# Kernel tuning notes

Hardware: AMD Instinct MI355X
Metric: run time of the kernel (lower is better)

## Reference

```python
import jax, jax.numpy as jnp
import numpy as np

N = 50000   # nodes
E = 800000  # edges (avg degree 16)
H = 3       # attention heads
D_IN, D_HID, D_OUT = 256, 64, 10


def setup_inputs() -> dict:
    key = jax.random.key(0)
    ks = jax.random.split(key, 8)
    x = jax.random.normal(ks[0], (N, D_IN), dtype=jnp.float32)
    edge_index = jax.random.randint(ks[1], (2, E), 0, N, dtype=jnp.int64)
    W1 = jax.random.normal(ks[2], (H, D_IN, D_HID), dtype=jnp.float32) / np.sqrt(D_IN)
    a_src1 = jax.random.normal(ks[3], (H, D_HID), dtype=jnp.float32) / np.sqrt(D_HID)
    a_dst1 = jax.random.normal(ks[4], (H, D_HID), dtype=jnp.float32) / np.sqrt(D_HID)
    W2 = jax.random.normal(ks[5], (H, D_HID, D_OUT), dtype=jnp.float32) / np.sqrt(D_HID)
    a_src2 = jax.random.normal(ks[6], (H, D_OUT), dtype=jnp.float32) / np.sqrt(D_OUT)
    a_dst2 = jax.random.normal(ks[7], (H, D_OUT), dtype=jnp.float32) / np.sqrt(D_OUT)
    return {"x": x, "edge_index": edge_index, "W1": W1, "a_src1": a_src1,
            "a_dst1": a_dst1, "W2": W2, "a_src2": a_src2, "a_dst2": a_dst2}


def gat_layer(x, src, dst, W, a_s, a_d, n):
    # x: [N, Din]; W: [H, Din, Dout]; returns [N, Dout] (heads averaged)
    z = jnp.einsum('nd,hde->nhe', x, W)                     # [N, H, Dout]
    e_src = jnp.einsum('nhe,he->nh', z, a_s)[src]           # [E, H]
    e_dst = jnp.einsum('nhe,he->nh', z, a_d)[dst]           # [E, H]
    e = jax.nn.leaky_relu(e_src + e_dst, 0.2)               # [E, H]
    # numerically-stable softmax over incoming edges of each dst node
    m = jax.lax.stop_gradient(jax.ops.segment_max(e, dst, num_segments=n))
    ex = jnp.exp(e - m[dst])                                # [E, H]
    denom = jax.ops.segment_sum(ex, dst, num_segments=n)    # [N, H]
    alpha = ex / (denom[dst] + 1e-16)                       # [E, H]
    out = jax.ops.segment_sum(z[src] * alpha[:, :, None], dst, num_segments=n)
    return out.mean(axis=1)                                 # [N, Dout]


def reference(x, edge_index, W1, a_src1, a_dst1, W2, a_src2, a_dst2):
    n = x.shape[0]
    src, dst = edge_index[0], edge_index[1]
    # dropout layers are identity in eval/deterministic mode
    h = gat_layer(x, src, dst, W1, a_src1, a_dst1, n)
    h = jax.nn.elu(h)
    h = gat_layer(h, src, dst, W2, a_src2, a_dst2, n)
    return h, jax.nn.log_softmax(h, axis=1)
```

## Files before the change

kernel.cpp:

```cpp
#include <hip/hip_runtime.h>
#include <math.h>

#define DIN  256
#define DHID 64
#define NH   3
#define DOUT 10
#define CAP  64

typedef __attribute__((ext_vector_type(8))) short bf16x8;
typedef __attribute__((ext_vector_type(4))) float f32x4;

__device__ inline unsigned short f2bf(float f) {
    unsigned u = __builtin_bit_cast(unsigned, f);
    unsigned r = (u + 0x7FFFu + ((u >> 16) & 1u)) >> 16;
    return (unsigned short)r;
}
__device__ inline float bf2f(unsigned short s) {
    unsigned u = ((unsigned)s) << 16;
    return __builtin_bit_cast(float, u);
}
__device__ inline f32x4 cvt4(ushort4 z) {
    f32x4 r;
    r[0] = bf2f(z.x); r[1] = bf2f(z.y); r[2] = bf2f(z.z); r[3] = bf2f(z.w);
    return r;
}


__global__ __launch_bounds__(256) void repack_zero_kernel(const float* __restrict__ W1,
                                                          const float* __restrict__ W2,
                                                          unsigned short* __restrict__ W1p,
                                                          float* __restrict__ W2cat,
                                                          int* __restrict__ cursor, int N) {
    int bid = blockIdx.x;
    int tid = threadIdx.x;
    int nzb = (N + 255) >> 8;
    if (bid < 192) {
        int idx = bid * 256 + tid;
        int j = idx & 7, l = (idx >> 3) & 63, q = (idx >> 9) & 7, t = idx >> 12;
        int c = t * 16 + (l & 15);
        int k = q * 32 + (l >> 4) * 8 + j;
        int h = c >> 6, jj = c & 63;
        W1p[idx] = f2bf(W1[h * 16384 + k * 64 + jj]);
    } else if (bid < 192 + nzb) {
        int i = (bid - 192) * 256 + tid;
        if (i < N) cursor[i] = 0;
    } else {
        int idx = (bid - 192 - nzb) * 256 + tid;
        if (idx < 2048) {
            int kk = idx >> 5, c = idx & 31;
            float wv = 0.f;
            if (c < 30) {
                int h = c / 10, j = c % 10;
                wv = W2[(h * 64 + kk) * 10 + j];
            }
            W2cat[idx] = wv;
        }
    }
}


#define SCHUNK 2048

__global__ __launch_bounds__(256) void scatter_kernel(const int* __restrict__ src,
                                                      const int* __restrict__ dst,
                                                      int* __restrict__ cursor,
                                                      unsigned short* __restrict__ esrcp,
                                                      int E, int pbase) {
    int part = blockIdx.x & 7;
    int base = (blockIdx.x >> 3) * SCHUNK;
    int tid = threadIdx.x;
    int lo = part * pbase, hi = lo + pbase;
    #pragma unroll
    for (int k = 0; k < SCHUNK / 256; ++k) {
        int i = base + k * 256 + tid;
        if (i < E) {
            int d = dst[i];
            int s = src[i];
            if (d >= lo && d < hi) {
                int pos = atomicAdd(cursor + d, 1);
                if (pos < CAP) esrcp[d * CAP + pos] = (unsigned short)s;
            }
        }
    }
}


__global__ __launch_bounds__(128) void gemm1_mfma_kernel(const float* __restrict__ x,
                                                         const bf16x8* __restrict__ W1p,
                                                         const float* __restrict__ a_s,
                                                         const float* __restrict__ a_d,
                                                         unsigned short* __restrict__ z1bf,
                                                         float* __restrict__ s1,
                                                         float* __restrict__ d1, int n) {
    __shared__ unsigned short Xs[32][272];
    int tid = threadIdx.x;
    int w = tid >> 6, lane = tid & 63;
    int m = lane & 15, quad = lane >> 4;
    int n0 = blockIdx.x * 32;

    for (int i = tid; i < 2048; i += 128) {
        int r = i >> 6, c4 = i & 63;
        int nn = n0 + r;
        float4 a = (nn < n) ? *(const float4*)(x + (size_t)nn * 256 + c4 * 4)
                            : (float4){0.f, 0.f, 0.f, 0.f};
        ushort4 b;
        b.x = f2bf(a.x); b.y = f2bf(a.y); b.z = f2bf(a.z); b.w = f2bf(a.w);
        *(ushort4*)(&Xs[r][c4 * 4]) = b;
    }
    __syncthreads();

    int rloc = w * 16 + m;
    f32x4 acc[12];
    #pragma unroll
    for (int t = 0; t < 12; ++t) acc[t] = (f32x4){0.f, 0.f, 0.f, 0.f};
    #pragma unroll
    for (int q = 0; q < 8; ++q) {
        bf16x8 af = *(const bf16x8*)(&Xs[rloc][q * 32 + quad * 8]);
        #pragma unroll
        for (int t = 0; t < 12; ++t) {
            bf16x8 bfr = W1p[(t * 8 + q) * 64 + lane];
            acc[t] = __builtin_amdgcn_mfma_f32_16x16x32_bf16(af, bfr, acc[t], 0, 0, 0);
        }
    }
    __syncthreads();

    float as_r[12], ad_r[12];
    #pragma unroll
    for (int t = 0; t < 12; ++t) { as_r[t] = a_s[t * 16 + m]; ad_r[t] = a_d[t * 16 + m]; }

    #pragma unroll
    for (int reg = 0; reg < 4; ++reg) {
        int row_loc = w * 16 + quad * 4 + reg;
        int row_out = n0 + row_loc;
        bool ok = row_out < n;
        float ps[3] = {0.f, 0.f, 0.f}, pd[3] = {0.f, 0.f, 0.f};
        #pragma unroll
        for (int t = 0; t < 12; ++t) {
            float v = acc[t][reg];
            Xs[row_loc][t * 16 + m] = f2bf(v);
            ps[t >> 2] += v * as_r[t];
            pd[t >> 2] += v * ad_r[t];
        }
        #pragma unroll
        for (int h = 0; h < 3; ++h) {
            float s = ps[h], d = pd[h];
            #pragma unroll
            for (int msk = 1; msk < 16; msk <<= 1) {
                s += __shfl_xor(s, msk, 16);
                d += __shfl_xor(d, msk, 16);
            }
            if (ok && m == 0) { s1[row_out * 4 + h] = s; d1[row_out * 4 + h] = d; }
        }
    }
    __syncthreads();

    for (int i = tid; i < 1536; i += 128) {
        int r = i / 48, c4 = i % 48;
        int nn = n0 + r;
        if (nn < n)
            *(ushort4*)(z1bf + (size_t)nn * 192 + c4 * 4) = *(const ushort4*)(&Xs[r][c4 * 4]);
    }
}


__global__ __launch_bounds__(256) void agg1_gemm2_kernel(
        const int* __restrict__ cnts, const unsigned short* __restrict__ esrcp,
        const float* __restrict__ s1, const float* __restrict__ d1,
        const unsigned short* __restrict__ z1bf,
        const float* __restrict__ W2cat, const float* __restrict__ as2,
        const float* __restrict__ ad2,
        unsigned short* __restrict__ z2bf,
        float* __restrict__ s2, float* __restrict__ d2, int n) {
    __shared__ float Ws[64][32];
    __shared__ float wlds[4][196];
    __shared__ float hb[4][64];
    __shared__ float tb[4][64];
    int tid = threadIdx.x;
    int lane = tid & 63, wave = tid >> 6;

    for (int idx = tid; idx < 1024; idx += 256)
        ((float2*)&Ws[0][0])[idx] = ((const float2*)W2cat)[idx];
    __syncthreads();

    int v = blockIdx.x * 4 + wave;
    if (v >= n) return;
    int cnt = cnts[v]; if (cnt > CAP) cnt = CAP;
    int m16 = lane & 15;
    int grp = lane >> 4;
    int head = grp > 2 ? 2 : grp;
    bool rowact = lane < 48;
    float dv0 = d1[v * 4], dv1 = d1[v * 4 + 1], dv2 = d1[v * 4 + 2];
    float* wl = wlds[wave];

    int u_l = 0; float w0 = 0.f, w1 = 0.f, w2 = 0.f;
    if (lane < cnt) {
        u_l = (int)esrcp[v * CAP + lane];
        float4 sv = *(const float4*)(s1 + (size_t)u_l * 4);
        float e0 = sv.x + dv0; e0 = e0 > 0.f ? e0 : 0.2f * e0;
        float e1 = sv.y + dv1; e1 = e1 > 0.f ? e1 : 0.2f * e1;
        float e2 = sv.z + dv2; e2 = e2 > 0.f ? e2 : 0.2f * e2;
        w0 = __expf(e0); w1 = __expf(e1); w2 = __expf(e2);
    }
    wl[lane] = w0; wl[65 + lane] = w1; wl[130 + lane] = w2;

    f32x4 acc = (f32x4){0.f, 0.f, 0.f, 0.f};
    if (rowact) {
        int rnd = (cnt + 7) & ~7;
        const int wb = head * 65;
        ushort4 zr[8]; float wr[8];
        #pragma unroll
        for (int i = 0; i < 8; ++i) {
            int u = __builtin_amdgcn_readlane(u_l, i);
            zr[i] = *(const ushort4*)(z1bf + (size_t)u * 192 + lane * 4);
            wr[i] = wl[wb + i];
        }
        for (int j = 8; j < rnd; j += 8) {
            ushort4 zn[8]; float wn[8];
            #pragma unroll
            for (int i = 0; i < 8; ++i) {
                int u = __builtin_amdgcn_readlane(u_l, j + i);
                zn[i] = *(const ushort4*)(z1bf + (size_t)u * 192 + lane * 4);
                wn[i] = wl[wb + j + i];
            }
            #pragma unroll
            for (int i = 0; i < 8; ++i) acc += cvt4(zr[i]) * wr[i];
            #pragma unroll
            for (int i = 0; i < 8; ++i) { zr[i] = zn[i]; wr[i] = wn[i]; }
        }
        #pragma unroll
        for (int i = 0; i < 8; ++i) acc += cvt4(zr[i]) * wr[i];
    }

    float4 wv4 = *(const float4*)(&wl[head * 65 + m16 * 4]);
    float denp = wv4.x + wv4.y + wv4.z + wv4.w;
    #pragma unroll
    for (int msk = 1; msk < 16; msk <<= 1) denp += __shfl_xor(denp, msk, 16);

    float invd = (1.f / 3.f) / (denp + 1e-16f);
    float acc0 = rowact ? acc[0] * invd : 0.f;
    float acc1 = rowact ? acc[1] * invd : 0.f;
    float acc2 = rowact ? acc[2] * invd : 0.f;
    float acc3 = rowact ? acc[3] * invd : 0.f;
    acc0 += __shfl_down(acc0, 32, 64); acc0 += __shfl_down(acc0, 16, 64);
    acc1 += __shfl_down(acc1, 32, 64); acc1 += __shfl_down(acc1, 16, 64);
    acc2 += __shfl_down(acc2, 32, 64); acc2 += __shfl_down(acc2, 16, 64);
    acc3 += __shfl_down(acc3, 32, 64); acc3 += __shfl_down(acc3, 16, 64);
    if (lane < 16) {
        float4 o;
        o.x = acc0 > 0.f ? acc0 : __expf(acc0) - 1.f;
        o.y = acc1 > 0.f ? acc1 : __expf(acc1) - 1.f;
        o.z = acc2 > 0.f ? acc2 : __expf(acc2) - 1.f;
        o.w = acc3 > 0.f ? acc3 : __expf(acc3) - 1.f;
        *(float4*)(&hb[wave][lane * 4]) = o;
    }

    int c = lane & 31, half = lane >> 5;
    int k0 = half * 32;
    float zc0 = 0.f, zc1 = 0.f;
    #pragma unroll
    for (int k = 0; k < 32; k += 2) {
        zc0 += hb[wave][k0 + k]     * Ws[k0 + k][c];
        zc1 += hb[wave][k0 + k + 1] * Ws[k0 + k + 1][c];
    }
    float zc = zc0 + zc1;
    zc += __shfl_down(zc, 32, 64);
    if (lane < 32) {
        z2bf[(size_t)v * 32 + c] = f2bf(zc);
        if (c < 30) {
            tb[wave][c]      = zc * as2[c];
            tb[wave][32 + c] = zc * ad2[c];
        }
    }
    if (lane < 6) {
        int h = lane >> 1;
        int base = (lane & 1) * 32 + h * 10;
        float sum = 0.f;
        #pragma unroll
        for (int j = 0; j < 10; ++j) sum += tb[wave][base + j];
        if ((lane & 1) == 0) s2[v * 4 + h] = sum;
        else                 d2[v * 4 + h] = sum;
    }
}


__global__ __launch_bounds__(256) void agg2_kernel(const int* __restrict__ cnts,
                                                   const unsigned short* __restrict__ esrcp,
                                                   const float* __restrict__ s2,
                                                   const float* __restrict__ d2,
                                                   const unsigned short* __restrict__ z2bf,
                                                   float* __restrict__ out, int n) {
    __shared__ float wlds[4][196];
    __shared__ float dlds[4][4];
    int tid = threadIdx.x;
    int lane = tid & 63, wave = tid >> 6;
    int v = blockIdx.x * 4 + wave;
    if (v >= n) return;
    int cnt = cnts[v]; if (cnt > CAP) cnt = CAP;
    int c2 = lane & 15;
    int quad = lane >> 4;
    int headc = c2 < 5 ? 0 : (c2 < 10 ? 1 : 2);
    int headg = quad > 2 ? 2 : quad;
    float dv0 = d2[v * 4], dv1 = d2[v * 4 + 1], dv2 = d2[v * 4 + 2];
    float* wl = wlds[wave];

    int u_l = 0; float w0 = 0.f, w1 = 0.f, w2 = 0.f;
    if (lane < cnt) {
        u_l = (int)esrcp[v * CAP + lane];
        float4 sv = *(const float4*)(s2 + (size_t)u_l * 4);
        float e0 = sv.x + dv0; e0 = e0 > 0.f ? e0 : 0.2f * e0;
        float e1 = sv.y + dv1; e1 = e1 > 0.f ? e1 : 0.2f * e1;
        float e2 = sv.z + dv2; e2 = e2 > 0.f ? e2 : 0.2f * e2;
        w0 = __expf(e0); w1 = __expf(e1); w2 = __expf(e2);
    }
    wl[lane] = w0; wl[65 + lane] = w1; wl[130 + lane] = w2;

    float ax = 0.f, ay = 0.f;
    {
        int rnd = (cnt + 7) & ~7;
        const int wb = headc * 65;
        int ua = __shfl(u_l, quad, 64);
        int ub = __shfl(u_l, 4 + quad, 64);
        float wa = wl[wb + quad], wbb = wl[wb + 4 + quad];
        ushort2 za = *(const ushort2*)(z2bf + (size_t)ua * 32 + c2 * 2);
        ushort2 zb = *(const ushort2*)(z2bf + (size_t)ub * 32 + c2 * 2);
        for (int j = 8; j < rnd; j += 8) {
            int un1 = __shfl(u_l, j + quad, 64);
            int un2 = __shfl(u_l, j + 4 + quad, 64);
            float wn1 = wl[wb + j + quad], wn2 = wl[wb + j + 4 + quad];
            ushort2 zn1 = *(const ushort2*)(z2bf + (size_t)un1 * 32 + c2 * 2);
            ushort2 zn2 = *(const ushort2*)(z2bf + (size_t)un2 * 32 + c2 * 2);
            ax += wa * bf2f(za.x) + wbb * bf2f(zb.x);
            ay += wa * bf2f(za.y) + wbb * bf2f(zb.y);
            wa = wn1; wbb = wn2; za = zn1; zb = zn2;
        }
        ax += wa * bf2f(za.x) + wbb * bf2f(zb.x);
        ay += wa * bf2f(za.y) + wbb * bf2f(zb.y);
    }

    float4 wv = *(const float4*)(&wl[headg * 65 + c2 * 4]);
    float denp = wv.x + wv.y + wv.z + wv.w;
    #pragma unroll
    for (int msk = 1; msk < 16; msk <<= 1) denp += __shfl_xor(denp, msk, 16);
    if (c2 == 0 && quad < 3) dlds[wave][quad] = denp;
    float den = dlds[wave][headc];

    ax += __shfl_down(ax, 32, 64); ax += __shfl_down(ax, 16, 64);
    ay += __shfl_down(ay, 32, 64); ay += __shfl_down(ay, 16, 64);
    float inv = 1.f / (den + 1e-16f);
    float rx = ax * inv, ry = ay * inv;
    float rx5  = __shfl(rx, lane + 5, 64);
    float rx10 = __shfl(rx, lane + 10, 64);
    float ry5  = __shfl(ry, lane + 5, 64);
    float ry10 = __shfl(ry, lane + 10, 64);
    float rrx = (rx + rx5 + rx10) * (1.f / 3.f);
    float rry = (ry + ry5 + ry10) * (1.f / 3.f);
    bool act = lane < 5;
    float mx = act ? fmaxf(rrx, rry) : -1e30f;
    #pragma unroll
    for (int msk = 1; msk < 8; msk <<= 1) mx = fmaxf(mx, __shfl_xor(mx, msk, 8));
    float e = act ? (__expf(rrx - mx) + __expf(rry - mx)) : 0.f;
    #pragma unroll
    for (int msk = 1; msk < 8; msk <<= 1) e += __shfl_xor(e, msk, 8);
    float lg = __logf(e);
    if (act) {
        float2 o1; o1.x = rrx; o1.y = rry;
        float2 o2; o2.x = rrx - mx - lg; o2.y = rry - mx - lg;
        *(float2*)(out + (size_t)v * DOUT + c2 * 2) = o1;
        *(float2*)(out + (size_t)n * DOUT + (size_t)v * DOUT + c2 * 2) = o2;
    }
}


extern "C" void kernel_launch(void* const* d_in, const int* in_sizes, int n_in,
                              void* d_out, int out_size, void* d_ws, size_t ws_size,
                              hipStream_t stream) {
    const float* x   = (const float*)d_in[0];
    const int*   ei  = (const int*)d_in[1];
    const float* W1  = (const float*)d_in[2];
    const float* as1 = (const float*)d_in[3];
    const float* ad1 = (const float*)d_in[4];
    const float* W2  = (const float*)d_in[5];
    const float* as2 = (const float*)d_in[6];
    const float* ad2 = (const float*)d_in[7];
    float* out = (float*)d_out;

    const int N = in_sizes[0] / DIN;
    const int E = in_sizes[1] / 2;
    const int* src = ei;
    const int* dst = ei + E;

    char* p = (char*)d_ws;
    auto alloc = [&](size_t bytes) -> void* {
        void* r = (void*)p;
        p += (bytes + 255) & ~(size_t)255;
        return r;
    };
    int* cursor  = (int*)alloc((size_t)N * 4);
    unsigned short* esrcp = (unsigned short*)alloc((size_t)N * CAP * 2);
    unsigned short* W1p  = (unsigned short*)alloc((size_t)49152 * 2);
    float* W2cat = (float*)alloc((size_t)2048 * 4);
    unsigned short* z1bf = (unsigned short*)alloc((size_t)N * 192 * 2);
    float* s1    = (float*)alloc((size_t)N * 4 * 4);
    float* d1    = (float*)alloc((size_t)N * 4 * 4);
    unsigned short* z2bf = (unsigned short*)alloc((size_t)N * 32 * 2);
    float* s2    = (float*)alloc((size_t)N * 4 * 4);
    float* d2    = (float*)alloc((size_t)N * 4 * 4);
    (void)alloc(512);

    int nzb = (N + 255) / 256;
    repack_zero_kernel<<<192 + nzb + 8, 256, 0, stream>>>(W1, W2, W1p, W2cat, cursor, N);

    int pbase = (N + 7) / 8;
    int nchunks = (E + SCHUNK - 1) / SCHUNK;
    scatter_kernel<<<nchunks * 8, 256, 0, stream>>>(src, dst, cursor, esrcp, E, pbase);

    gemm1_mfma_kernel<<<(N + 31) / 32, 128, 0, stream>>>(x, (const bf16x8*)W1p, as1, ad1,
                                                         z1bf, s1, d1, N);
    agg1_gemm2_kernel<<<(N + 3) / 4, 256, 0, stream>>>(cursor, esrcp, s1, d1, z1bf,
                                                       W2cat, as2, ad2, z2bf, s2, d2, N);
    agg2_kernel<<<(N + 3) / 4, 256, 0, stream>>>(cursor, esrcp, s2, d2, z2bf, out, N);
}
```

Baseline: 248.6 us.

## Deepen gather prefetch in agg1 and keep transposed W2 in registers

The fused layer-1 aggregation and layer-2 GEMM kernel now issues the first 16 neighbour-row gathers before computing the attention weights, and keeps two batches of 8 in flight instead of one. It also drops the per-block shared-memory staging of W2 and its __syncthreads, loading a transposed W2 layout straight into registers as float4 vectors. The per-wave weight buffer is padded to a 68-float stride so weights can be read as vector loads. In exchange register pressure rises and every node now processes at least 16 neighbour slots, even when it has fewer.

```diff
diff --git a/kernel.cpp b/kernel.cpp
--- a/kernel.cpp
+++ b/kernel.cpp
@@ -29,7 +29,7 @@
 __global__ __launch_bounds__(256) void repack_zero_kernel(const float* __restrict__ W1,
                                                           const float* __restrict__ W2,
                                                           unsigned short* __restrict__ W1p,
-                                                          float* __restrict__ W2cat,
+                                                          float* __restrict__ W2catT,
                                                           int* __restrict__ cursor, int N) {
     int bid = blockIdx.x;
     int tid = threadIdx.x;
@@ -47,13 +47,13 @@
     } else {
         int idx = (bid - 192 - nzb) * 256 + tid;
         if (idx < 2048) {
-            int kk = idx >> 5, c = idx & 31;
+            int cc = idx >> 6, kk = idx & 63;
             float wv = 0.f;
-            if (c < 30) {
-                int h = c / 10, j = c % 10;
+            if (cc < 30) {
+                int h = cc / 10, j = cc % 10;
                 wv = W2[(h * 64 + kk) * 10 + j];
             }
-            W2cat[idx] = wv;
+            W2catT[idx] = wv;
         }
     }
 }
@@ -163,76 +163,94 @@
 }
 
 
+#define CONSUME8(Z, OFF)                                              \
+    {                                                                 \
+        f32x4 wa4 = *(const f32x4*)(&wl[wb + (OFF)]);                 \
+        f32x4 wb4 = *(const f32x4*)(&wl[wb + (OFF) + 4]);             \
+        acc += cvt4(Z[0]) * wa4[0]; acc += cvt4(Z[1]) * wa4[1];       \
+        acc += cvt4(Z[2]) * wa4[2]; acc += cvt4(Z[3]) * wa4[3];       \
+        acc += cvt4(Z[4]) * wb4[0]; acc += cvt4(Z[5]) * wb4[1];       \
+        acc += cvt4(Z[6]) * wb4[2]; acc += cvt4(Z[7]) * wb4[3];       \
+    }
+
 __global__ __launch_bounds__(256) void agg1_gemm2_kernel(
         const int* __restrict__ cnts, const unsigned short* __restrict__ esrcp,
         const float* __restrict__ s1, const float* __restrict__ d1,
         const unsigned short* __restrict__ z1bf,
-        const float* __restrict__ W2cat, const float* __restrict__ as2,
+        const float* __restrict__ W2catT, const float* __restrict__ as2,
         const float* __restrict__ ad2,
         unsigned short* __restrict__ z2bf,
         float* __restrict__ s2, float* __restrict__ d2, int n) {
-    __shared__ float Ws[64][32];
-    __shared__ float wlds[4][196];
+    __shared__ float wlds[4][204];
     __shared__ float hb[4][64];
     __shared__ float tb[4][64];
     int tid = threadIdx.x;
     int lane = tid & 63, wave = tid >> 6;
-
-    for (int idx = tid; idx < 1024; idx += 256)
-        ((float2*)&Ws[0][0])[idx] = ((const float2*)W2cat)[idx];
-    __syncthreads();
-
     int v = blockIdx.x * 4 + wave;
     if (v >= n) return;
     int cnt = cnts[v]; if (cnt > CAP) cnt = CAP;
     int m16 = lane & 15;
     int grp = lane >> 4;
     int head = grp > 2 ? 2 : grp;
+    int c = lane & 31, half = lane >> 5;
     bool rowact = lane < 48;
+    const int wb = head * 68;
+    float* wl = wlds[wave];
+
+    int u_l = 0;
+    if (lane < cnt) u_l = (int)esrcp[v * CAP + lane];
+
+    ushort4 zA[8], zB[8];
+    if (rowact) {
+        #pragma unroll
+        for (int i = 0; i < 8; ++i) {
+            int u = __builtin_amdgcn_readlane(u_l, i);
+            zA[i] = *(const ushort4*)(z1bf + (size_t)u * 192 + lane * 4);
+        }
+        #pragma unroll
+        for (int i = 0; i < 8; ++i) {
+            int u = __builtin_amdgcn_readlane(u_l, 8 + i);
+            zB[i] = *(const ushort4*)(z1bf + (size_t)u * 192 + lane * 4);
+        }
+    }
+
+    f32x4 wsr[8];
+    #pragma unroll
+    for (int j2 = 0; j2 < 8; ++j2)
+        wsr[j2] = *(const f32x4*)(W2catT + (c << 6) + (half << 5) + (j2 << 2));
+
     float dv0 = d1[v * 4], dv1 = d1[v * 4 + 1], dv2 = d1[v * 4 + 2];
-    float* wl = wlds[wave];
-
-    int u_l = 0; float w0 = 0.f, w1 = 0.f, w2 = 0.f;
+    float w0 = 0.f, w1 = 0.f, w2 = 0.f;
     if (lane < cnt) {
-        u_l = (int)esrcp[v * CAP + lane];
         float4 sv = *(const float4*)(s1 + (size_t)u_l * 4);
         float e0 = sv.x + dv0; e0 = e0 > 0.f ? e0 : 0.2f * e0;
         float e1 = sv.y + dv1; e1 = e1 > 0.f ? e1 : 0.2f * e1;
         float e2 = sv.z + dv2; e2 = e2 > 0.f ? e2 : 0.2f * e2;
         w0 = __expf(e0); w1 = __expf(e1); w2 = __expf(e2);
     }
-    wl[lane] = w0; wl[65 + lane] = w1; wl[130 + lane] = w2;
-
+    wl[lane] = w0; wl[68 + lane] = w1; wl[136 + lane] = w2;
+
+    int rnd = (cnt + 7) & ~7; if (rnd < 16) rnd = 16;
     f32x4 acc = (f32x4){0.f, 0.f, 0.f, 0.f};
     if (rowact) {
-        int rnd = (cnt + 7) & ~7;
-        const int wb = head * 65;
-        ushort4 zr[8]; float wr[8];
-        #pragma unroll
-        for (int i = 0; i < 8; ++i) {
-            int u = __builtin_amdgcn_readlane(u_l, i);
-            zr[i] = *(const ushort4*)(z1bf + (size_t)u * 192 + lane * 4);
-            wr[i] = wl[wb + i];
-        }
-        for (int j = 8; j < rnd; j += 8) {
-            ushort4 zn[8]; float wn[8];
+        int jc = 0;
+        for (int js = 16; js < rnd; js += 8) {
+            ushort4 zN[8];
             #pragma unroll
             for (int i = 0; i < 8; ++i) {
-                int u = __builtin_amdgcn_readlane(u_l, j + i);
-                zn[i] = *(const ushort4*)(z1bf + (size_t)u * 192 + lane * 4);
-                wn[i] = wl[wb + j + i];
+                int u = __builtin_amdgcn_readlane(u_l, js + i);
+                zN[i] = *(const ushort4*)(z1bf + (size_t)u * 192 + lane * 4);
             }
+            CONSUME8(zA, jc); jc += 8;
             #pragma unroll
-            for (int i = 0; i < 8; ++i) acc += cvt4(zr[i]) * wr[i];
-            #pragma unroll
-            for (int i = 0; i < 8; ++i) { zr[i] = zn[i]; wr[i] = wn[i]; }
-        }
-        #pragma unroll
-        for (int i = 0; i < 8; ++i) acc += cvt4(zr[i]) * wr[i];
-    }
-
-    float4 wv4 = *(const float4*)(&wl[head * 65 + m16 * 4]);
-    float denp = wv4.x + wv4.y + wv4.z + wv4.w;
+            for (int i = 0; i < 8; ++i) { zA[i] = zB[i]; zB[i] = zN[i]; }
+        }
+        CONSUME8(zA, jc);
+        CONSUME8(zB, jc + 8);
+    }
+
+    f32x4 wv4 = *(const f32x4*)(&wl[head * 68 + m16 * 4]);
+    float denp = wv4[0] + wv4[1] + wv4[2] + wv4[3];
     #pragma unroll
     for (int msk = 1; msk < 16; msk <<= 1) denp += __shfl_xor(denp, msk, 16);
 
@@ -254,15 +272,13 @@
         *(float4*)(&hb[wave][lane * 4]) = o;
     }
 
-    int c = lane & 31, half = lane >> 5;
-    int k0 = half * 32;
-    float zc0 = 0.f, zc1 = 0.f;
-    #pragma unroll
-    for (int k = 0; k < 32; k += 2) {
-        zc0 += hb[wave][k0 + k]     * Ws[k0 + k][c];
-        zc1 += hb[wave][k0 + k + 1] * Ws[k0 + k + 1][c];
-    }
-    float zc = zc0 + zc1;
+    f32x4 accW = (f32x4){0.f, 0.f, 0.f, 0.f};
+    #pragma unroll
+    for (int j2 = 0; j2 < 8; ++j2) {
+        f32x4 h4 = *(const f32x4*)(&hb[wave][(half << 5) + (j2 << 2)]);
+        accW += h4 * wsr[j2];
+    }
+    float zc = accW[0] + accW[1] + accW[2] + accW[3];
     zc += __shfl_down(zc, 32, 64);
     if (lane < 32) {
         z2bf[(size_t)v * 32 + c] = f2bf(zc);
@@ -398,7 +414,7 @@
     int* cursor  = (int*)alloc((size_t)N * 4);
     unsigned short* esrcp = (unsigned short*)alloc((size_t)N * CAP * 2);
     unsigned short* W1p  = (unsigned short*)alloc((size_t)49152 * 2);
-    float* W2cat = (float*)alloc((size_t)2048 * 4);
+    float* W2catT = (float*)alloc((size_t)2048 * 4);
     unsigned short* z1bf = (unsigned short*)alloc((size_t)N * 192 * 2);
     float* s1    = (float*)alloc((size_t)N * 4 * 4);
     float* d1    = (float*)alloc((size_t)N * 4 * 4);
@@ -408,7 +424,7 @@
     (void)alloc(512);
 
     int nzb = (N + 255) / 256;
-    repack_zero_kernel<<<192 + nzb + 8, 256, 0, stream>>>(W1, W2, W1p, W2cat, cursor, N);
+    repack_zero_kernel<<<192 + nzb + 8, 256, 0, stream>>>(W1, W2, W1p, W2catT, cursor, N);
 
     int pbase = (N + 7) / 8;
     int nchunks = (E + SCHUNK - 1) / SCHUNK;
@@ -417,6 +433,6 @@
     gemm1_mfma_kernel<<<(N + 31) / 32, 128, 0, stream>>>(x, (const bf16x8*)W1p, as1, ad1,
                                                          z1bf, s1, d1, N);
     agg1_gemm2_kernel<<<(N + 3) / 4, 256, 0, stream>>>(cursor, esrcp, s1, d1, z1bf,
-                                                       W2cat, as2, ad2, z2bf, s2, d2, N);
+                                                       W2catT, as2, ad2, z2bf, s2, d2, N);
     agg2_kernel<<<(N + 3) / 4, 256, 0, stream>>>(cursor, esrcp, s2, d2, z2bf, out, N);
 }
```

Result: slower. 275.6 us (+10.9%).

## Split each node's layer-1 aggregation across two waves and combine via LDS

Applied to the files above, without the earlier changes.

The layer-1 aggregation kernel now gives each destination node two waves, each gathering half of its incoming edges. The second wave writes its partial accumulators and softmax denominator to shared memory, and the first wave combines them and runs the fused ELU plus second-layer projection. This doubles the grid and halves the per-wave serial gather chain, exposing more memory-level parallelism at the cost of a block barrier and an idle half-wave during the epilogue. The scatter kernel also loads src only for edges that fall in the block's partition.

```diff
diff --git a/kernel.cpp b/kernel.cpp
--- a/kernel.cpp
+++ b/kernel.cpp
@@ -75,8 +75,8 @@
         int i = base + k * 256 + tid;
         if (i < E) {
             int d = dst[i];
-            int s = src[i];
             if (d >= lo && d < hi) {
+                int s = src[i];
                 int pos = atomicAdd(cursor + d, 1);
                 if (pos < CAP) esrcp[d * CAP + pos] = (unsigned short)s;
             }
@@ -172,41 +172,46 @@
         unsigned short* __restrict__ z2bf,
         float* __restrict__ s2, float* __restrict__ d2, int n) {
     __shared__ float Ws[64][32];
-    __shared__ float wlds[4][196];
-    __shared__ float hb[4][64];
-    __shared__ float tb[4][64];
+    __shared__ float wlds[4][102];
+    __shared__ float accb[2][200];
+    __shared__ float hb[2][64];
+    __shared__ float tb[2][64];
     int tid = threadIdx.x;
     int lane = tid & 63, wave = tid >> 6;
 
     for (int idx = tid; idx < 1024; idx += 256)
         ((float2*)&Ws[0][0])[idx] = ((const float2*)W2cat)[idx];
-    __syncthreads();
-
-    int v = blockIdx.x * 4 + wave;
-    if (v >= n) return;
+
+    int pairid = wave >> 1;
+    int hf = wave & 1;
+    int v = blockIdx.x * 2 + pairid;
+    if (v >= n) v = n - 1;
     int cnt = cnts[v]; if (cnt > CAP) cnt = CAP;
+    int cnt2 = (cnt + 1) >> 1;
+    int myoff = hf * cnt2;
+    int mycnt = hf ? (cnt - cnt2) : cnt2;
     int m16 = lane & 15;
     int grp = lane >> 4;
     int head = grp > 2 ? 2 : grp;
     bool rowact = lane < 48;
+    const int wb = head * 34;
+    float* wl = wlds[wave];
+
     float dv0 = d1[v * 4], dv1 = d1[v * 4 + 1], dv2 = d1[v * 4 + 2];
-    float* wl = wlds[wave];
-
     int u_l = 0; float w0 = 0.f, w1 = 0.f, w2 = 0.f;
-    if (lane < cnt) {
-        u_l = (int)esrcp[v * CAP + lane];
+    if (lane < mycnt) {
+        u_l = (int)esrcp[v * CAP + myoff + lane];
         float4 sv = *(const float4*)(s1 + (size_t)u_l * 4);
         float e0 = sv.x + dv0; e0 = e0 > 0.f ? e0 : 0.2f * e0;
         float e1 = sv.y + dv1; e1 = e1 > 0.f ? e1 : 0.2f * e1;
         float e2 = sv.z + dv2; e2 = e2 > 0.f ? e2 : 0.2f * e2;
         w0 = __expf(e0); w1 = __expf(e1); w2 = __expf(e2);
     }
-    wl[lane] = w0; wl[65 + lane] = w1; wl[130 + lane] = w2;
+    if (lane < 32) { wl[lane] = w0; wl[34 + lane] = w1; wl[68 + lane] = w2; }
 
     f32x4 acc = (f32x4){0.f, 0.f, 0.f, 0.f};
     if (rowact) {
-        int rnd = (cnt + 7) & ~7;
-        const int wb = head * 65;
+        int rnd = (mycnt + 7) & ~7;
         ushort4 zr[8]; float wr[8];
         #pragma unroll
         for (int i = 0; i < 8; ++i) {
@@ -231,54 +236,63 @@
         for (int i = 0; i < 8; ++i) acc += cvt4(zr[i]) * wr[i];
     }
 
-    float4 wv4 = *(const float4*)(&wl[head * 65 + m16 * 4]);
-    float denp = wv4.x + wv4.y + wv4.z + wv4.w;
+    float2 dpr = *(const float2*)(&wl[head * 34 + m16 * 2]);
+    float denp = dpr.x + dpr.y;
     #pragma unroll
     for (int msk = 1; msk < 16; msk <<= 1) denp += __shfl_xor(denp, msk, 16);
 
-    float invd = (1.f / 3.f) / (denp + 1e-16f);
-    float acc0 = rowact ? acc[0] * invd : 0.f;
-    float acc1 = rowact ? acc[1] * invd : 0.f;
-    float acc2 = rowact ? acc[2] * invd : 0.f;
-    float acc3 = rowact ? acc[3] * invd : 0.f;
-    acc0 += __shfl_down(acc0, 32, 64); acc0 += __shfl_down(acc0, 16, 64);
-    acc1 += __shfl_down(acc1, 32, 64); acc1 += __shfl_down(acc1, 16, 64);
-    acc2 += __shfl_down(acc2, 32, 64); acc2 += __shfl_down(acc2, 16, 64);
-    acc3 += __shfl_down(acc3, 32, 64); acc3 += __shfl_down(acc3, 16, 64);
-    if (lane < 16) {
-        float4 o;
-        o.x = acc0 > 0.f ? acc0 : __expf(acc0) - 1.f;
-        o.y = acc1 > 0.f ? acc1 : __expf(acc1) - 1.f;
-        o.z = acc2 > 0.f ? acc2 : __expf(acc2) - 1.f;
-        o.w = acc3 > 0.f ? acc3 : __expf(acc3) - 1.f;
-        *(float4*)(&hb[wave][lane * 4]) = o;
-    }
-
-    int c = lane & 31, half = lane >> 5;
-    int k0 = half * 32;
-    float zc0 = 0.f, zc1 = 0.f;
-    #pragma unroll
-    for (int k = 0; k < 32; k += 2) {
-        zc0 += hb[wave][k0 + k]     * Ws[k0 + k][c];
-        zc1 += hb[wave][k0 + k + 1] * Ws[k0 + k + 1][c];
-    }
-    float zc = zc0 + zc1;
-    zc += __shfl_down(zc, 32, 64);
-    if (lane < 32) {
-        z2bf[(size_t)v * 32 + c] = f2bf(zc);
-        if (c < 30) {
-            tb[wave][c]      = zc * as2[c];
-            tb[wave][32 + c] = zc * ad2[c];
-        }
-    }
-    if (lane < 6) {
-        int h = lane >> 1;
-        int base = (lane & 1) * 32 + h * 10;
-        float sum = 0.f;
-        #pragma unroll
-        for (int j = 0; j < 10; ++j) sum += tb[wave][base + j];
-        if ((lane & 1) == 0) s2[v * 4 + h] = sum;
-        else                 d2[v * 4 + h] = sum;
+    if (hf) {
+        if (rowact) *(f32x4*)(&accb[pairid][lane * 4]) = acc;
+        if (m16 == 0 && grp < 3) accb[pairid][192 + grp] = denp;
+    }
+    __syncthreads();
+    if (hf == 0) {
+        if (rowact) acc += *(const f32x4*)(&accb[pairid][lane * 4]);
+        float den = denp + accb[pairid][192 + head];
+        float invd = (1.f / 3.f) / (den + 1e-16f);
+        float acc0 = rowact ? acc[0] * invd : 0.f;
+        float acc1 = rowact ? acc[1] * invd : 0.f;
+        float acc2 = rowact ? acc[2] * invd : 0.f;
+        float acc3 = rowact ? acc[3] * invd : 0.f;
+        acc0 += __shfl_down(acc0, 32, 64); acc0 += __shfl_down(acc0, 16, 64);
+        acc1 += __shfl_down(acc1, 32, 64); acc1 += __shfl_down(acc1, 16, 64);
+        acc2 += __shfl_down(acc2, 32, 64); acc2 += __shfl_down(acc2, 16, 64);
+        acc3 += __shfl_down(acc3, 32, 64); acc3 += __shfl_down(acc3, 16, 64);
+        if (lane < 16) {
+            float4 o;
+            o.x = acc0 > 0.f ? acc0 : __expf(acc0) - 1.f;
+            o.y = acc1 > 0.f ? acc1 : __expf(acc1) - 1.f;
+            o.z = acc2 > 0.f ? acc2 : __expf(acc2) - 1.f;
+            o.w = acc3 > 0.f ? acc3 : __expf(acc3) - 1.f;
+            *(float4*)(&hb[pairid][lane * 4]) = o;
+        }
+
+        int c = lane & 31, half = lane >> 5;
+        int k0 = half * 32;
+        float zc0 = 0.f, zc1 = 0.f;
+        #pragma unroll
+        for (int k = 0; k < 32; k += 2) {
+            zc0 += hb[pairid][k0 + k]     * Ws[k0 + k][c];
+            zc1 += hb[pairid][k0 + k + 1] * Ws[k0 + k + 1][c];
+        }
+        float zc = zc0 + zc1;
+        zc += __shfl_down(zc, 32, 64);
+        if (lane < 32) {
+            z2bf[(size_t)v * 32 + c] = f2bf(zc);
+            if (c < 30) {
+                tb[pairid][c]      = zc * as2[c];
+                tb[pairid][32 + c] = zc * ad2[c];
+            }
+        }
+        if (lane < 6) {
+            int h = lane >> 1;
+            int base = (lane & 1) * 32 + h * 10;
+            float sum = 0.f;
+            #pragma unroll
+            for (int j = 0; j < 10; ++j) sum += tb[pairid][base + j];
+            if ((lane & 1) == 0) s2[v * 4 + h] = sum;
+            else                 d2[v * 4 + h] = sum;
+        }
     }
 }
 
@@ -416,7 +430,7 @@
 
     gemm1_mfma_kernel<<<(N + 31) / 32, 128, 0, stream>>>(x, (const bf16x8*)W1p, as1, ad1,
                                                          z1bf, s1, d1, N);
-    agg1_gemm2_kernel<<<(N + 3) / 4, 256, 0, stream>>>(cursor, esrcp, s1, d1, z1bf,
+    agg1_gemm2_kernel<<<(N + 1) / 2, 256, 0, stream>>>(cursor, esrcp, s1, d1, z1bf,
                                                        W2cat, as2, ad2, z2bf, s2, d2, N);
     agg2_kernel<<<(N + 3) / 4, 256, 0, stream>>>(cursor, esrcp, s2, d2, z2bf, out, N);
 }
```

Result: slower. 272.1 us (+9.5%).
